# Kernel optimization log

Hardware: AMD Instinct MI355X
Metric: run time of the kernel (lower is better)

The kernel has to match this reference:

```python
import jax, jax.numpy as jnp
import numpy as np

N = 50_000      # num_nodes
E = 1_600_000   # num_edges
R = 8           # num_relations
D = 128         # hidden_dim
L = 3           # num_layers
EPS = 1e-5


def setup_inputs() -> dict:
    key = jax.random.key(0)
    ks = jax.random.split(key, 10)
    x = jnp.arange(N, dtype=jnp.int64) if jax.config.jax_enable_x64 else jnp.arange(N, dtype=jnp.int32)
    edge_index = jax.random.randint(ks[0], (2, E), 0, N)
    edge_type = jax.random.randint(ks[1], (E,), 0, R)
    emb = jax.random.normal(ks[2], (N, D), dtype=jnp.float32) * (1.0 / np.sqrt(D))
    w_rel = jax.random.normal(ks[3], (L, R, D, D), dtype=jnp.float32) * (1.0 / np.sqrt(D))
    w_root = jax.random.normal(ks[4], (L, D, D), dtype=jnp.float32) * (1.0 / np.sqrt(D))
    bias = jax.random.normal(ks[5], (L, D), dtype=jnp.float32) * 0.01
    gamma = 1.0 + 0.1 * jax.random.normal(ks[6], (L, D), dtype=jnp.float32)
    beta = 0.1 * jax.random.normal(ks[7], (L, D), dtype=jnp.float32)
    return {"x": x, "edge_index": edge_index, "edge_type": edge_type,
            "emb": emb, "w_rel": w_rel, "w_root": w_root, "bias": bias,
            "gamma": gamma, "beta": beta}


def _layer_norm(h, g, b):
    mu = jnp.mean(h, axis=-1, keepdims=True)
    var = jnp.mean(jnp.square(h - mu), axis=-1, keepdims=True)
    return (h - mu) * jax.lax.rsqrt(var + EPS) * g + b


def _rgcn_conv(h, src, dst, etype, w_rel, w_root, b):
    # PyG RGCNConv: per-relation mean aggregation of transformed neighbors + root transform + bias
    hr = jnp.einsum('nd,rdf->rnf', h, w_rel)          # [R, N, D] relation-transformed features
    msg = hr[etype, src]                               # [E, D] gather per edge
    seg = etype * N + dst                              # combined (relation, target) segment id
    sums = jax.ops.segment_sum(msg, seg, num_segments=R * N)            # [R*N, D]
    cnt = jax.ops.segment_sum(jnp.ones((msg.shape[0],), h.dtype), seg, num_segments=R * N)
    mean = sums / jnp.maximum(cnt, 1.0)[:, None]
    agg = mean.reshape(R, N, D).sum(axis=0)            # sum over relations
    return agg + h @ w_root + b


def reference(x, edge_index, edge_type, emb, w_rel, w_root, bias, gamma, beta):
    src, dst = edge_index[0], edge_index[1]
    h = emb[x]                                         # node embedding lookup
    for i in range(L):
        h_new = _rgcn_conv(h, src, dst, edge_type, w_rel[i], w_root[i], bias[i])
        h_new = jax.nn.relu(_layer_norm(h_new, gamma[i], beta[i]))
        # dropout is identity in eval/reference mode
        h = h + h_new if i > 0 else h_new
    return h
```

## Files before the change

kernel.cpp:

```cpp
#include <hip/hip_runtime.h>

#define NN 50000
#define NE 1600000
#define NR 8
#define ND 128
#define NL 3
#define RN (NR * NN)
#define LN_EPS 1e-5f
#define PADF 132

#define NBKT 196
#define BSH 11
#define STRIDE_PB 10240
#define STAGE_BYTES (NBKT * STRIDE_PB * 4)
#define BIN_BLOCKS 500
#define EPB 3200
#define I4PB 800

#define PREP_G (NN * 64)
#define PREP_W (27 * 16384)
#define PREP_TOT (PREP_G + PREP_W + NBKT)

#define WS_H    0
#define WS_ROW  14400000
#define WS_ADJ  16004096
#define WS_WB   22404096
#define WS_BIG  23288832
#define WS_NEED_NEW (23288832ULL + 9ULL * NN * 256)

typedef __attribute__((ext_vector_type(8))) short short8;
typedef __attribute__((ext_vector_type(4))) float float4v;
typedef __attribute__((ext_vector_type(4))) unsigned uint4v;

__device__ __forceinline__ float bflo(unsigned u) { return __uint_as_float(u << 16); }
__device__ __forceinline__ float bfhi(unsigned u) { return __uint_as_float(u & 0xFFFF0000u); }
__device__ __forceinline__ unsigned f2bf(float f) {
    unsigned u = __float_as_uint(f);
    return (u + 0x7FFFu + ((u >> 16) & 1u)) >> 16;
}
__device__ __forceinline__ unsigned pack2(float lo, float hi) {
    return f2bf(lo) | (f2bf(hi) << 16);
}

__global__ __launch_bounds__(256) void k_prep0(const int* __restrict__ x,
                                               const float* __restrict__ emb,
                                               const float* __restrict__ w_rel,
                                               const float* __restrict__ w_root,
                                               unsigned* __restrict__ h,
                                               unsigned short* __restrict__ wb,
                                               int* __restrict__ bcur) {
    int i = blockIdx.x * 256 + threadIdx.x;
    if (i < PREP_G) {
        int n = i >> 6, dw = i & 63;
        float2 v = *(const float2*)&emb[(size_t)x[n] * ND + 2 * dw];
        h[i] = pack2(v.x, v.y);
        return;
    }
    i -= PREP_G;
    if (i < PREP_W) {
        int m = i >> 14;
        int idx = i & 16383;
        int j = idx & 7;
        int lane = (idx >> 3) & 63;
        int ft = (idx >> 9) & 7;
        int kk = idx >> 12;
        int row = kk * 32 + (lane >> 4) * 8 + j;
        int col = ft * 16 + (lane & 15);
        const float* W = (m < 24) ? (w_rel + (size_t)m * 16384)
                                  : (w_root + (size_t)(m - 24) * 16384);
        wb[i] = (unsigned short)f2bf(W[row * ND + col]);
        return;
    }
    i -= PREP_W;
    if (i < NBKT) bcur[i] = 0;
}

__global__ __launch_bounds__(256) void k_binA(const int* __restrict__ src,
                                              const int* __restrict__ dst,
                                              const int* __restrict__ et,
                                              int* __restrict__ bcur,
                                              unsigned* __restrict__ stage) {
    __shared__ int lcnt[256];
    __shared__ int loff[256];
    __shared__ int lcur[256];
    __shared__ int sbase[256];
    __shared__ int tmp[256];
    __shared__ unsigned srt[EPB];
    __shared__ unsigned char bkt[EPB];

    int tid = threadIdx.x;
    lcnt[tid] = 0;
    __syncthreads();

    int base4 = blockIdx.x * I4PB;
    const int4* s4p = (const int4*)src;
    const int4* d4p = (const int4*)dst;
    const int4* t4p = (const int4*)et;

    for (int i4 = tid; i4 < I4PB; i4 += 256) {
        int4 d4 = d4p[base4 + i4];
        int4 t4 = t4p[base4 + i4];
        atomicAdd(&lcnt[(t4.x * NN + d4.x) >> BSH], 1);
        atomicAdd(&lcnt[(t4.y * NN + d4.y) >> BSH], 1);
        atomicAdd(&lcnt[(t4.z * NN + d4.z) >> BSH], 1);
        atomicAdd(&lcnt[(t4.w * NN + d4.w) >> BSH], 1);
    }
    __syncthreads();
    int own = lcnt[tid];
    tmp[tid] = own;
    __syncthreads();
    for (int off = 1; off < 256; off <<= 1) {
        int v = (tid >= off) ? tmp[tid - off] : 0;
        __syncthreads();
        tmp[tid] += v;
        __syncthreads();
    }
    int excl = tmp[tid] - own;
    loff[tid] = excl;
    lcur[tid] = excl;
    if (tid < NBKT) sbase[tid] = atomicAdd(&bcur[tid], own);
    __syncthreads();

    for (int i4 = tid; i4 < I4PB; i4 += 256) {
        int4 s4 = s4p[base4 + i4];
        int4 d4 = d4p[base4 + i4];
        int4 t4 = t4p[base4 + i4];
        int segs[4] = {t4.x * NN + d4.x, t4.y * NN + d4.y,
                       t4.z * NN + d4.z, t4.w * NN + d4.w};
        int srcs[4] = {s4.x, s4.y, s4.z, s4.w};
#pragma unroll
        for (int j = 0; j < 4; j++) {
            int seg = segs[j];
            int b = seg >> BSH;
            unsigned rec = ((unsigned)(seg & 2047) << 16) | (unsigned)srcs[j];
            int pos = atomicAdd(&lcur[b], 1);
            srt[pos] = rec;
            bkt[pos] = (unsigned char)b;
        }
    }
    __syncthreads();
    for (int i = tid; i < EPB; i += 256) {
        int b = bkt[i];
        stage[(size_t)b * STRIDE_PB + sbase[b] + (i - loff[b])] = srt[i];
    }
}

__global__ __launch_bounds__(256) void k_binB(const unsigned* __restrict__ stage,
                                              const int* __restrict__ bcur,
                                              int* __restrict__ rowstart,
                                              int* __restrict__ adj) {
    __shared__ int tmp[256];
    __shared__ int lcnt2[2048];
    __shared__ int loff2[2048];
    __shared__ unsigned short srt2[STRIDE_PB];
    __shared__ int gbase_s, n_s;

    int tid = threadIdx.x;
    int b = blockIdx.x;

    int bv = (tid < NBKT) ? bcur[tid] : 0;
    tmp[tid] = bv;
    __syncthreads();
    for (int off = 1; off < 256; off <<= 1) {
        int v = (tid >= off) ? tmp[tid - off] : 0;
        __syncthreads();
        tmp[tid] += v;
        __syncthreads();
    }
    if (tid == b) { gbase_s = tmp[tid] - bv; n_s = bv; }
    for (int j = tid; j < 2048; j += 256) lcnt2[j] = 0;
    __syncthreads();

    int n = n_s;
    const unsigned* sp = stage + (size_t)b * STRIDE_PB;
    for (int i = tid; i < n; i += 256)
        atomicAdd(&lcnt2[sp[i] >> 16], 1);
    __syncthreads();

    int v8[8];
    int s8 = 0;
    int base8 = tid * 8;
#pragma unroll
    for (int j = 0; j < 8; j++) { v8[j] = lcnt2[base8 + j]; s8 += v8[j]; }
    tmp[tid] = s8;
    __syncthreads();
    for (int off = 1; off < 256; off <<= 1) {
        int v = (tid >= off) ? tmp[tid - off] : 0;
        __syncthreads();
        tmp[tid] += v;
        __syncthreads();
    }
    int run = tmp[tid] - s8;
#pragma unroll
    for (int j = 0; j < 8; j++) { loff2[base8 + j] = run; run += v8[j]; }
    __syncthreads();
    for (int j = tid; j < 2048; j += 256) lcnt2[j] = loff2[j];
    __syncthreads();

    for (int i = tid; i < n; i += 256) {
        unsigned rec = sp[i];
        int pos = atomicAdd(&lcnt2[rec >> 16], 1);
        srt2[pos] = (unsigned short)(rec & 0xFFFFu);
    }
    __syncthreads();

    int gb = gbase_s;
    for (int i = tid; i < n; i += 256) adj[gb + i] = (int)srt2[i];
    int segbase = b << BSH;
    for (int j = tid; j < 2048; j += 256) {
        int seg = segbase + j;
        if (seg < RN) rowstart[seg] = gb + loff2[j];
    }
    if (b == NBKT - 1 && tid == 0) rowstart[RN] = NE;
}


__global__ __launch_bounds__(256) void k_mm(const unsigned* __restrict__ h32,
                                            const unsigned short* __restrict__ wrel,
                                            const unsigned short* __restrict__ wroot,
                                            unsigned* __restrict__ hr) {
    __shared__ uint4 SB4[2048];
    __shared__ unsigned TR[4][16][66];
    const unsigned short* SBs = (const unsigned short*)SB4;

    int tid = threadIdx.x;
    int wave = tid >> 6, lane = tid & 63;
    int quad = lane >> 4, l15 = lane & 15;
    int w0w = blockIdx.x * 64 + wave * 16;
    int gi = w0w + l15; gi = gi < NN ? gi : NN - 1;
    int pr = l15 & 1;

    const unsigned* Hrow = h32 + (size_t)gi * 64;
    short8 afr[4];
#pragma unroll
    for (int kk = 0; kk < 4; kk++)
        afr[kk] = *(const short8*)&Hrow[kk * 16 + quad * 4];

    for (int m = 0; m < 9; m++) {
        const unsigned short* W = (m < 8) ? (wrel + (size_t)m * 16384) : wroot;
        __syncthreads();
        {
            const uint4* Wg = (const uint4*)W;
#pragma unroll
            for (int i = 0; i < 8; i++) SB4[tid + 256 * i] = Wg[tid + 256 * i];
        }
        __syncthreads();

        float4v acc[8];
#pragma unroll
        for (int i = 0; i < 8; i++) acc[i] = (float4v){0.f, 0.f, 0.f, 0.f};
#pragma unroll
        for (int kk = 0; kk < 4; kk++) {
#pragma unroll
            for (int ft = 0; ft < 8; ft++) {
                short8 bf = *(const short8*)&SBs[((kk * 8 + ft) * 64 + lane) * 8];
                acc[ft] = __builtin_amdgcn_mfma_f32_16x16x32_bf16(afr[kk], bf, acc[ft], 0, 0, 0);
            }
        }

#pragma unroll
        for (int ft = 0; ft < 8; ft++) {
            float4v part;
#pragma unroll
            for (int rg = 0; rg < 4; rg++) part[rg] = __shfl_xor(acc[ft][rg], 1, 64);
            if ((ft & 1) == pr) {
                int a = l15 >> 1;
#pragma unroll
                for (int rg = 0; rg < 4; rg++) {
                    float lo = pr ? part[rg] : acc[ft][rg];
                    float hi = pr ? acc[ft][rg] : part[rg];
                    TR[wave][quad * 4 + rg][ft * 8 + a] = pack2(lo, hi);
                }
            }
        }
        unsigned* hrm = hr + (size_t)m * NN * 64;
#pragma unroll
        for (int ps = 0; ps < 4; ps++) {
            int ri = ps * 4 + quad;
            uint4 v = *(const uint4*)&TR[wave][ri][l15 * 4];
            int row = w0w + ri;
            if (row < NN)
                *(uint4*)&hrm[(size_t)row * 64 + l15 * 4] = v;
        }
    }
}

#define AGA(u)                                  \
    a0 += bflo(u.x); a1 += bfhi(u.x);           \
    a2 += bflo(u.y); a3 += bfhi(u.y);           \
    a4 += bflo(u.z); a5 += bfhi(u.z);           \
    a6 += bflo(u.w); a7 += bfhi(u.w);
#define AGC(u)                                  \
    c0 += bflo(u.x); c1 += bfhi(u.x);           \
    c2 += bflo(u.y); c3 += bfhi(u.y);           \
    c4 += bflo(u.z); c5 += bfhi(u.z);           \
    c6 += bflo(u.w); c7 += bfhi(u.w);

__global__ __launch_bounds__(256) void k_aggln(const unsigned* __restrict__ hr,
                                               unsigned* __restrict__ h32,
                                               const int* __restrict__ adj,
                                               const int* __restrict__ rowstart,
                                               const float* __restrict__ bias,
                                               const float* __restrict__ gamma,
                                               const float* __restrict__ beta,
                                               float* __restrict__ out_f,
                                               int add_res, int last) {
    int n = (blockIdx.x * 256 + threadIdx.x) >> 4;
    int l15 = threadIdx.x & 15;

    float t0 = 0.f, t1 = 0.f, t2 = 0.f, t3 = 0.f,
          t4 = 0.f, t5 = 0.f, t6 = 0.f, t7 = 0.f;

    for (int r = 0; r < NR; r++) {
        int seg = r * NN + n;
        int st = rowstart[seg], en = rowstart[seg + 1];
        st = st < 0 ? 0 : st;
        en = en > NE ? NE : en;
        const unsigned* T = hr + (size_t)r * NN * 64;

        float a0 = 0.f, a1 = 0.f, a2 = 0.f, a3 = 0.f,
              a4 = 0.f, a5 = 0.f, a6 = 0.f, a7 = 0.f;
        float c0 = 0.f, c1 = 0.f, c2 = 0.f, c3 = 0.f,
              c4 = 0.f, c5 = 0.f, c6 = 0.f, c7 = 0.f;
        int p = st;
        for (; p + 3 < en; p += 4) {
            unsigned s0 = (unsigned)adj[p],     s1 = (unsigned)adj[p + 1];
            unsigned s2 = (unsigned)adj[p + 2], s3 = (unsigned)adj[p + 3];
            s0 = s0 < NN ? s0 : NN - 1;
            s1 = s1 < NN ? s1 : NN - 1;
            s2 = s2 < NN ? s2 : NN - 1;
            s3 = s3 < NN ? s3 : NN - 1;
            uint4 u0 = *(const uint4*)&T[(size_t)s0 * 64 + l15 * 4];
            uint4 u1 = *(const uint4*)&T[(size_t)s1 * 64 + l15 * 4];
            uint4 u2 = *(const uint4*)&T[(size_t)s2 * 64 + l15 * 4];
            uint4 u3 = *(const uint4*)&T[(size_t)s3 * 64 + l15 * 4];
            AGA(u0) AGC(u1) AGA(u2) AGC(u3)
        }
        for (; p < en; p++) {
            unsigned s0 = (unsigned)adj[p];
            s0 = s0 < NN ? s0 : NN - 1;
            uint4 u0 = *(const uint4*)&T[(size_t)s0 * 64 + l15 * 4];
            AGA(u0)
        }
        int d = en - st;
        float sc = 1.0f / (float)(d > 1 ? d : 1);
        t0 += (a0 + c0) * sc; t1 += (a1 + c1) * sc;
        t2 += (a2 + c2) * sc; t3 += (a3 + c3) * sc;
        t4 += (a4 + c4) * sc; t5 += (a5 + c5) * sc;
        t6 += (a6 + c6) * sc; t7 += (a7 + c7) * sc;
    }

    {
        uint4 u = *(const uint4*)&hr[((size_t)8 * NN + n) * 64 + l15 * 4];
        t0 += bflo(u.x); t1 += bfhi(u.x);
        t2 += bflo(u.y); t3 += bfhi(u.y);
        t4 += bflo(u.z); t5 += bfhi(u.z);
        t6 += bflo(u.w); t7 += bfhi(u.w);
    }
    int f0 = 8 * l15;
    {
        float4 b0 = *(const float4*)&bias[f0];
        float4 b1 = *(const float4*)&bias[f0 + 4];
        t0 += b0.x; t1 += b0.y; t2 += b0.z; t3 += b0.w;
        t4 += b1.x; t5 += b1.y; t6 += b1.z; t7 += b1.w;
    }

    float s = t0 + t1 + t2 + t3 + t4 + t5 + t6 + t7;
#pragma unroll
    for (int off = 1; off < 16; off <<= 1) s += __shfl_xor(s, off, 64);
    float mu = s * (1.0f / ND);
    float e0 = t0 - mu, e1 = t1 - mu, e2 = t2 - mu, e3 = t3 - mu,
          e4 = t4 - mu, e5 = t5 - mu, e6 = t6 - mu, e7 = t7 - mu;
    float vs = e0 * e0 + e1 * e1 + e2 * e2 + e3 * e3 +
               e4 * e4 + e5 * e5 + e6 * e6 + e7 * e7;
#pragma unroll
    for (int off = 1; off < 16; off <<= 1) vs += __shfl_xor(vs, off, 64);
    float rr = rsqrtf(vs * (1.0f / ND) + LN_EPS);

    float4 g0 = *(const float4*)&gamma[f0];
    float4 g1 = *(const float4*)&gamma[f0 + 4];
    float4 be0 = *(const float4*)&beta[f0];
    float4 be1 = *(const float4*)&beta[f0 + 4];
    float o0 = fmaxf(e0 * rr * g0.x + be0.x, 0.0f);
    float o1 = fmaxf(e1 * rr * g0.y + be0.y, 0.0f);
    float o2 = fmaxf(e2 * rr * g0.z + be0.z, 0.0f);
    float o3 = fmaxf(e3 * rr * g0.w + be0.w, 0.0f);
    float o4 = fmaxf(e4 * rr * g1.x + be1.x, 0.0f);
    float o5 = fmaxf(e5 * rr * g1.y + be1.y, 0.0f);
    float o6 = fmaxf(e6 * rr * g1.z + be1.z, 0.0f);
    float o7 = fmaxf(e7 * rr * g1.w + be1.w, 0.0f);

    if (add_res) {
        uint4 u = *(const uint4*)&h32[(size_t)n * 64 + l15 * 4];
        o0 += bflo(u.x); o1 += bfhi(u.x);
        o2 += bflo(u.y); o3 += bfhi(u.y);
        o4 += bflo(u.z); o5 += bfhi(u.z);
        o6 += bflo(u.w); o7 += bfhi(u.w);
    }
    if (last) {
        *(float4*)&out_f[(size_t)n * ND + f0] = make_float4(o0, o1, o2, o3);
        *(float4*)&out_f[(size_t)n * ND + f0 + 4] = make_float4(o4, o5, o6, o7);
    } else {
        uint4 w;
        w.x = pack2(o0, o1); w.y = pack2(o2, o3);
        w.z = pack2(o4, o5); w.w = pack2(o6, o7);
        *(uint4*)&h32[(size_t)n * 64 + l15 * 4] = w;
    }
}


__global__ __launch_bounds__(256) void k_agg(const unsigned* __restrict__ h32,
                                             const int* __restrict__ adj,
                                             const int* __restrict__ rowstart,
                                             unsigned* __restrict__ S) {
    int q = (blockIdx.x * 256 + threadIdx.x) >> 4;
    int l15 = threadIdx.x & 15;
    int r = q / NN;
    int n = q - r * NN;
    int st = rowstart[q], en = rowstart[q + 1];
    st = st < 0 ? 0 : st;
    en = en > NE ? NE : en;
    float a0 = 0.f, a1 = 0.f, a2 = 0.f, a3 = 0.f,
          a4 = 0.f, a5 = 0.f, a6 = 0.f, a7 = 0.f;
    float c0 = 0.f, c1 = 0.f, c2 = 0.f, c3 = 0.f,
          c4 = 0.f, c5 = 0.f, c6 = 0.f, c7 = 0.f;
    int p = st;
    for (; p + 3 < en; p += 4) {
        unsigned s0 = (unsigned)adj[p],     s1 = (unsigned)adj[p + 1];
        unsigned s2 = (unsigned)adj[p + 2], s3 = (unsigned)adj[p + 3];
        s0 = s0 < NN ? s0 : NN - 1;
        s1 = s1 < NN ? s1 : NN - 1;
        s2 = s2 < NN ? s2 : NN - 1;
        s3 = s3 < NN ? s3 : NN - 1;
        uint4 u0 = *(const uint4*)&h32[(size_t)s0 * 64 + l15 * 4];
        uint4 u1 = *(const uint4*)&h32[(size_t)s1 * 64 + l15 * 4];
        uint4 u2 = *(const uint4*)&h32[(size_t)s2 * 64 + l15 * 4];
        uint4 u3 = *(const uint4*)&h32[(size_t)s3 * 64 + l15 * 4];
        AGA(u0) AGC(u1) AGA(u2) AGC(u3)
    }
    for (; p < en; p++) {
        unsigned s0 = (unsigned)adj[p];
        s0 = s0 < NN ? s0 : NN - 1;
        uint4 u0 = *(const uint4*)&h32[(size_t)s0 * 64 + l15 * 4];
        AGA(u0)
    }
    int d = en - st;
    float sc = 1.0f / (float)(d > 1 ? d : 1);
    a0 = (a0 + c0) * sc; a1 = (a1 + c1) * sc;
    a2 = (a2 + c2) * sc; a3 = (a3 + c3) * sc;
    a4 = (a4 + c4) * sc; a5 = (a5 + c5) * sc;
    a6 = (a6 + c6) * sc; a7 = (a7 + c7) * sc;
    uint4v w;
    w.x = pack2(a0, a1); w.y = pack2(a2, a3);
    w.z = pack2(a4, a5); w.w = pack2(a6, a7);
    __builtin_nontemporal_store(w, (uint4v*)&S[(size_t)n * 512 + r * 64 + l15 * 4]);
}

__global__ __launch_bounds__(256) void k_gemm(const unsigned* __restrict__ S,
                                              unsigned* __restrict__ h32,
                                              const unsigned short* __restrict__ wrel,
                                              const unsigned short* __restrict__ wroot,
                                              const float* __restrict__ bias,
                                              const float* __restrict__ gamma,
                                              const float* __restrict__ beta,
                                              float* __restrict__ out_f,
                                              int add_res, int last) {
    __shared__ char smraw[4 * 16 * PADF * 4];
    float* SLF = (float*)smraw;
    uint4* SB4 = (uint4*)smraw;
    const unsigned short* SBs = (const unsigned short*)smraw;

    int tid = threadIdx.x;
    int wave = tid >> 6, lane = tid & 63;
    int quad = lane >> 4, l15 = lane & 15;
    int w0 = blockIdx.x * 64 + wave * 16;
    int gi = w0 + l15; gi = gi < NN ? gi : NN - 1;
    float* WF = SLF + wave * 16 * PADF;

    float4v acc[8];
#pragma unroll
    for (int i = 0; i < 8; i++) acc[i] = (float4v){0.f, 0.f, 0.f, 0.f};

    const unsigned* Sr = S + (size_t)gi * 512;
    for (int r = 0; r < NR; r++) {
        short8 afr[4];
#pragma unroll
        for (int kk = 0; kk < 4; kk++)
            afr[kk] = *(const short8*)&Sr[r * 64 + kk * 16 + quad * 4];
        __syncthreads();
        {
            const uint4* Wg = (const uint4*)(wrel + (size_t)r * 16384);
#pragma unroll
            for (int i = 0; i < 8; i++) SB4[tid + 256 * i] = Wg[tid + 256 * i];
        }
        __syncthreads();
#pragma unroll
        for (int kk = 0; kk < 4; kk++) {
#pragma unroll
            for (int ft = 0; ft < 8; ft++) {
                short8 bf = *(const short8*)&SBs[((kk * 8 + ft) * 64 + lane) * 8];
                acc[ft] = __builtin_amdgcn_mfma_f32_16x16x32_bf16(afr[kk], bf, acc[ft], 0, 0, 0);
            }
        }
    }
    {
        const unsigned* Hr = h32 + (size_t)gi * 64;
        short8 afr[4];
#pragma unroll
        for (int kk = 0; kk < 4; kk++)
            afr[kk] = *(const short8*)&Hr[kk * 16 + quad * 4];
        __syncthreads();
        {
            const uint4* Wg = (const uint4*)wroot;
#pragma unroll
            for (int i = 0; i < 8; i++) SB4[tid + 256 * i] = Wg[tid + 256 * i];
        }
        __syncthreads();
#pragma unroll
        for (int kk = 0; kk < 4; kk++) {
#pragma unroll
            for (int ft = 0; ft < 8; ft++) {
                short8 bf = *(const short8*)&SBs[((kk * 8 + ft) * 64 + lane) * 8];
                acc[ft] = __builtin_amdgcn_mfma_f32_16x16x32_bf16(afr[kk], bf, acc[ft], 0, 0, 0);
            }
        }
    }
    __syncthreads();

#pragma unroll
    for (int ft = 0; ft < 8; ft++)
#pragma unroll
        for (int rg = 0; rg < 4; rg++)
            WF[(quad * 4 + rg) * PADF + ft * 16 + l15] = acc[ft][rg];

    float2 bia = *(const float2*)&bias[2 * lane];
    float2 gam = *(const float2*)&gamma[2 * lane];
    float2 bet = *(const float2*)&beta[2 * lane];

    for (int i = 0; i < 16; i++) {
        int g = w0 + i;
        if (g >= NN) continue;
        float v0 = WF[i * PADF + 2 * lane] + bia.x;
        float v1 = WF[i * PADF + 2 * lane + 1] + bia.y;
        float s = v0 + v1;
#pragma unroll
        for (int off = 32; off > 0; off >>= 1) s += __shfl_xor(s, off, 64);
        float mu = s * (1.0f / ND);
        float e0 = v0 - mu, e1 = v1 - mu;
        float vs = e0 * e0 + e1 * e1;
#pragma unroll
        for (int off = 32; off > 0; off >>= 1) vs += __shfl_xor(vs, off, 64);
        float rr = rsqrtf(vs * (1.0f / ND) + LN_EPS);
        float o0 = fmaxf(e0 * rr * gam.x + bet.x, 0.0f);
        float o1 = fmaxf(e1 * rr * gam.y + bet.y, 0.0f);
        if (add_res) {
            unsigned u = h32[(size_t)g * 64 + lane];
            o0 += bflo(u);
            o1 += bfhi(u);
        }
        if (last) {
            *(float2*)&out_f[(size_t)g * ND + 2 * lane] = make_float2(o0, o1);
        } else {
            h32[(size_t)g * 64 + lane] = pack2(o0, o1);
        }
    }
}

extern "C" void kernel_launch(void* const* d_in, const int* in_sizes, int n_in,
                              void* d_out, int out_size, void* d_ws, size_t ws_size,
                              hipStream_t stream) {
    const int*   x      = (const int*)d_in[0];
    const int*   ei     = (const int*)d_in[1];
    const int*   et     = (const int*)d_in[2];
    const float* emb    = (const float*)d_in[3];
    const float* w_rel  = (const float*)d_in[4];
    const float* w_root = (const float*)d_in[5];
    const float* bias   = (const float*)d_in[6];
    const float* gamma  = (const float*)d_in[7];
    const float* beta   = (const float*)d_in[8];
    float* out = (float*)d_out;

    char* ws = (char*)d_ws;
    unsigned* h        = (unsigned*)(ws + WS_H);
    int*      rowstart = (int*)     (ws + WS_ROW);
    int*      adj      = (int*)     (ws + WS_ADJ);
    unsigned short* wb = (unsigned short*)(ws + WS_WB);
    unsigned* big      = (unsigned*)(ws + WS_BIG);
    unsigned* stage    = big;
    int*      bcur     = (int*)     (ws + WS_BIG + STAGE_BYTES);

    const int* src = ei;
    const int* dst = ei + NE;

    k_prep0<<<(PREP_TOT + 255) / 256, 256, 0, stream>>>(x, emb, w_rel, w_root,
                                                        h, wb, bcur);
    k_binA<<<BIN_BLOCKS, 256, 0, stream>>>(src, dst, et, bcur, stage);
    k_binB<<<NBKT, 256, 0, stream>>>(stage, bcur, rowstart, adj);

    if (ws_size >= WS_NEED_NEW) {
        for (int l = 0; l < NL; l++) {
            k_mm<<<(NN + 63) / 64, 256, 0, stream>>>(
                h, wb + (size_t)l * 8 * 16384, wb + (size_t)(24 + l) * 16384, big);
            k_aggln<<<NN * 16 / 256, 256, 0, stream>>>(
                big, h, adj, rowstart,
                bias + l * ND, gamma + l * ND, beta + l * ND,
                out, l > 0, l == NL - 1);
        }
    } else {
        for (int l = 0; l < NL; l++) {
            k_agg<<<RN * 16 / 256, 256, 0, stream>>>(h, adj, rowstart, big);
            k_gemm<<<(NN + 63) / 64, 256, 0, stream>>>(
                big, h,
                wb + (size_t)l * 8 * 16384, wb + (size_t)(24 + l) * 16384,
                bias + l * ND, gamma + l * ND, beta + l * ND,
                out, l > 0, l == NL - 1);
        }
    }
}
```

Measured before the change: 510.8 us.

## Merge prep with binning and first-layer GEMM with CSR finalize to cut launches

Folds the embedding/weight conversion blocks into the edge-binning kernel and runs the second binning pass alongside the first layer's relation GEMM in one launch, so independent work overlaps and kernel launches drop. Staging now lives in the output buffer with bcur zeroed by memset, and bounds clamps on source indices in the aggregation loops are removed with a 2-wide tail added. This adds overflow guards on stage indices and relies on input indices being in range.

```diff
diff --git a/kernel.cpp b/kernel.cpp
--- a/kernel.cpp
+++ b/kernel.cpp
@@ -12,17 +12,19 @@
 #define NBKT 196
 #define BSH 11
 #define STRIDE_PB 10240
-#define STAGE_BYTES (NBKT * STRIDE_PB * 4)
 #define BIN_BLOCKS 500
 #define EPB 3200
 #define I4PB 800
+#define MM_BLOCKS ((NN + 63) / 64)
 
 #define PREP_G (NN * 64)
 #define PREP_W (27 * 16384)
-#define PREP_TOT (PREP_G + PREP_W + NBKT)
+#define PREP_TOT (PREP_G + PREP_W)
+#define PREP_BLOCKS ((PREP_TOT + 255) / 256)
 
 #define WS_H    0
 #define WS_ROW  14400000
+#define WS_BCUR 16000064
 #define WS_ADJ  16004096
 #define WS_WB   22404096
 #define WS_BIG  23288832
@@ -42,44 +44,17 @@
     return f2bf(lo) | (f2bf(hi) << 16);
 }
 
-__global__ __launch_bounds__(256) void k_prep0(const int* __restrict__ x,
-                                               const float* __restrict__ emb,
-                                               const float* __restrict__ w_rel,
-                                               const float* __restrict__ w_root,
-                                               unsigned* __restrict__ h,
-                                               unsigned short* __restrict__ wb,
-                                               int* __restrict__ bcur) {
-    int i = blockIdx.x * 256 + threadIdx.x;
-    if (i < PREP_G) {
-        int n = i >> 6, dw = i & 63;
-        float2 v = *(const float2*)&emb[(size_t)x[n] * ND + 2 * dw];
-        h[i] = pack2(v.x, v.y);
-        return;
-    }
-    i -= PREP_G;
-    if (i < PREP_W) {
-        int m = i >> 14;
-        int idx = i & 16383;
-        int j = idx & 7;
-        int lane = (idx >> 3) & 63;
-        int ft = (idx >> 9) & 7;
-        int kk = idx >> 12;
-        int row = kk * 32 + (lane >> 4) * 8 + j;
-        int col = ft * 16 + (lane & 15);
-        const float* W = (m < 24) ? (w_rel + (size_t)m * 16384)
-                                  : (w_root + (size_t)(m - 24) * 16384);
-        wb[i] = (unsigned short)f2bf(W[row * ND + col]);
-        return;
-    }
-    i -= PREP_W;
-    if (i < NBKT) bcur[i] = 0;
-}
-
-__global__ __launch_bounds__(256) void k_binA(const int* __restrict__ src,
-                                              const int* __restrict__ dst,
-                                              const int* __restrict__ et,
-                                              int* __restrict__ bcur,
-                                              unsigned* __restrict__ stage) {
+__global__ __launch_bounds__(256) void k_prepbin(const int* __restrict__ x,
+                                                 const float* __restrict__ emb,
+                                                 const float* __restrict__ w_rel,
+                                                 const float* __restrict__ w_root,
+                                                 const int* __restrict__ src,
+                                                 const int* __restrict__ dst,
+                                                 const int* __restrict__ et,
+                                                 unsigned* __restrict__ h,
+                                                 unsigned short* __restrict__ wb,
+                                                 int* __restrict__ bcur,
+                                                 unsigned* __restrict__ stage) {
     __shared__ int lcnt[256];
     __shared__ int loff[256];
     __shared__ int lcur[256];
@@ -89,6 +64,31 @@
     __shared__ unsigned char bkt[EPB];
 
     int tid = threadIdx.x;
+    if (blockIdx.x >= BIN_BLOCKS) {
+        int i = (blockIdx.x - BIN_BLOCKS) * 256 + tid;
+        if (i < PREP_G) {
+            int n = i >> 6, dw = i & 63;
+            float2 v = *(const float2*)&emb[(size_t)x[n] * ND + 2 * dw];
+            h[i] = pack2(v.x, v.y);
+            return;
+        }
+        i -= PREP_G;
+        if (i < PREP_W) {
+            int m = i >> 14;
+            int idx = i & 16383;
+            int j = idx & 7;
+            int lane = (idx >> 3) & 63;
+            int ft = (idx >> 9) & 7;
+            int kk = idx >> 12;
+            int row = kk * 32 + (lane >> 4) * 8 + j;
+            int col = ft * 16 + (lane & 15);
+            const float* W = (m < 24) ? (w_rel + (size_t)m * 16384)
+                                      : (w_root + (size_t)(m - 24) * 16384);
+            wb[i] = (unsigned short)f2bf(W[row * ND + col]);
+        }
+        return;
+    }
+
     lcnt[tid] = 0;
     __syncthreads();
 
@@ -141,23 +141,19 @@
     __syncthreads();
     for (int i = tid; i < EPB; i += 256) {
         int b = bkt[i];
-        stage[(size_t)b * STRIDE_PB + sbase[b] + (i - loff[b])] = srt[i];
-    }
-}
-
-__global__ __launch_bounds__(256) void k_binB(const unsigned* __restrict__ stage,
-                                              const int* __restrict__ bcur,
-                                              int* __restrict__ rowstart,
-                                              int* __restrict__ adj) {
-    __shared__ int tmp[256];
-    __shared__ int lcnt2[2048];
-    __shared__ int loff2[2048];
-    __shared__ unsigned short srt2[STRIDE_PB];
-    __shared__ int gbase_s, n_s;
-
-    int tid = threadIdx.x;
-    int b = blockIdx.x;
-
+        int idx = sbase[b] + (i - loff[b]);
+        if (idx < STRIDE_PB)
+            stage[(size_t)b * STRIDE_PB + idx] = srt[i];
+    }
+}
+
+__device__ __forceinline__ void binB_body(const unsigned* __restrict__ stage,
+                                          const int* __restrict__ bcur,
+                                          int* __restrict__ rowstart,
+                                          int* __restrict__ adj,
+                                          int b, int tid,
+                                          int* tmp, int* lcnt2, int* loff2,
+                                          unsigned short* srt2, int* misc) {
     int bv = (tid < NBKT) ? bcur[tid] : 0;
     tmp[tid] = bv;
     __syncthreads();
@@ -167,11 +163,12 @@
         tmp[tid] += v;
         __syncthreads();
     }
-    if (tid == b) { gbase_s = tmp[tid] - bv; n_s = bv; }
+    if (tid == b) { misc[0] = tmp[tid] - bv; misc[1] = bv; }
     for (int j = tid; j < 2048; j += 256) lcnt2[j] = 0;
     __syncthreads();
 
-    int n = n_s;
+    int n = misc[1];
+    n = n < STRIDE_PB ? n : STRIDE_PB;
     const unsigned* sp = stage + (size_t)b * STRIDE_PB;
     for (int i = tid; i < n; i += 256)
         atomicAdd(&lcnt2[sp[i] >> 16], 1);
@@ -204,7 +201,7 @@
     }
     __syncthreads();
 
-    int gb = gbase_s;
+    int gb = misc[0];
     for (int i = tid; i < n; i += 256) adj[gb + i] = (int)srt2[i];
     int segbase = b << BSH;
     for (int j = tid; j < 2048; j += 256) {
@@ -214,75 +211,122 @@
     if (b == NBKT - 1 && tid == 0) rowstart[RN] = NE;
 }
 
+typedef unsigned TRarr[16][66];
+
+__device__ __forceinline__ void mm_body(const unsigned* __restrict__ h32,
+                                        const unsigned short* __restrict__ wrel,
+                                        const unsigned short* __restrict__ wroot,
+                                        unsigned* __restrict__ hr,
+                                        int mb, int tid,
+                                        uint4* SB4, TRarr* TRp) {
+    const unsigned short* SBs = (const unsigned short*)SB4;
+    int wave = tid >> 6, lane = tid & 63;
+    int quad = lane >> 4, l15 = lane & 15;
+    int w0w = mb * 64 + wave * 16;
+    int gi = w0w + l15; gi = gi < NN ? gi : NN - 1;
+    int pr = l15 & 1;
+
+    const unsigned* Hrow = h32 + (size_t)gi * 64;
+    short8 afr[4];
+#pragma unroll
+    for (int kk = 0; kk < 4; kk++)
+        afr[kk] = *(const short8*)&Hrow[kk * 16 + quad * 4];
+
+    for (int m = 0; m < 9; m++) {
+        const unsigned short* W = (m < 8) ? (wrel + (size_t)m * 16384) : wroot;
+        __syncthreads();
+        {
+            const uint4* Wg = (const uint4*)W;
+#pragma unroll
+            for (int i = 0; i < 8; i++) SB4[tid + 256 * i] = Wg[tid + 256 * i];
+        }
+        __syncthreads();
+
+        float4v acc[8];
+#pragma unroll
+        for (int i = 0; i < 8; i++) acc[i] = (float4v){0.f, 0.f, 0.f, 0.f};
+#pragma unroll
+        for (int kk = 0; kk < 4; kk++) {
+#pragma unroll
+            for (int ft = 0; ft < 8; ft++) {
+                short8 bf = *(const short8*)&SBs[((kk * 8 + ft) * 64 + lane) * 8];
+                acc[ft] = __builtin_amdgcn_mfma_f32_16x16x32_bf16(afr[kk], bf, acc[ft], 0, 0, 0);
+            }
+        }
+
+#pragma unroll
+        for (int ft = 0; ft < 8; ft++) {
+            float4v part;
+#pragma unroll
+            for (int rg = 0; rg < 4; rg++) part[rg] = __shfl_xor(acc[ft][rg], 1, 64);
+            if ((ft & 1) == pr) {
+                int a = l15 >> 1;
+#pragma unroll
+                for (int rg = 0; rg < 4; rg++) {
+                    float lo = pr ? part[rg] : acc[ft][rg];
+                    float hi = pr ? acc[ft][rg] : part[rg];
+                    TRp[wave][quad * 4 + rg][ft * 8 + a] = pack2(lo, hi);
+                }
+            }
+        }
+        unsigned* hrm = hr + (size_t)m * NN * 64;
+#pragma unroll
+        for (int ps = 0; ps < 4; ps++) {
+            int ri = ps * 4 + quad;
+            uint4 v = *(const uint4*)&TRp[wave][ri][l15 * 4];
+            int row = w0w + ri;
+            if (row < NN)
+                *(uint4*)&hrm[(size_t)row * 64 + l15 * 4] = v;
+        }
+    }
+}
+
+__global__ __launch_bounds__(256) void k_binB_mm(const unsigned* __restrict__ stage,
+                                                 const int* __restrict__ bcur,
+                                                 int* __restrict__ rowstart,
+                                                 int* __restrict__ adj,
+                                                 const unsigned* __restrict__ h32,
+                                                 const unsigned short* __restrict__ wrel,
+                                                 const unsigned short* __restrict__ wroot,
+                                                 unsigned* __restrict__ hr) {
+    __shared__ uint4 SMEM[3104];
+    int tid = threadIdx.x;
+    if (blockIdx.x < NBKT) {
+        int* tmp = (int*)SMEM;
+        int* lcnt2 = (int*)SMEM + 256;
+        int* loff2 = (int*)SMEM + 2304;
+        unsigned short* srt2 = (unsigned short*)((int*)SMEM + 4352);
+        int* misc = (int*)SMEM + 9472;
+        binB_body(stage, bcur, rowstart, adj, blockIdx.x, tid,
+                  tmp, lcnt2, loff2, srt2, misc);
+    } else {
+        mm_body(h32, wrel, wroot, hr, blockIdx.x - NBKT, tid,
+                SMEM, (TRarr*)(SMEM + 2048));
+    }
+}
+
+__global__ __launch_bounds__(256) void k_binB(const unsigned* __restrict__ stage,
+                                              const int* __restrict__ bcur,
+                                              int* __restrict__ rowstart,
+                                              int* __restrict__ adj) {
+    __shared__ uint4 SMEM[2369];
+    int tid = threadIdx.x;
+    int* tmp = (int*)SMEM;
+    int* lcnt2 = (int*)SMEM + 256;
+    int* loff2 = (int*)SMEM + 2304;
+    unsigned short* srt2 = (unsigned short*)((int*)SMEM + 4352);
+    int* misc = (int*)SMEM + 9472;
+    binB_body(stage, bcur, rowstart, adj, blockIdx.x, tid,
+              tmp, lcnt2, loff2, srt2, misc);
+}
 
 __global__ __launch_bounds__(256) void k_mm(const unsigned* __restrict__ h32,
                                             const unsigned short* __restrict__ wrel,
                                             const unsigned short* __restrict__ wroot,
                                             unsigned* __restrict__ hr) {
-    __shared__ uint4 SB4[2048];
-    __shared__ unsigned TR[4][16][66];
-    const unsigned short* SBs = (const unsigned short*)SB4;
-
-    int tid = threadIdx.x;
-    int wave = tid >> 6, lane = tid & 63;
-    int quad = lane >> 4, l15 = lane & 15;
-    int w0w = blockIdx.x * 64 + wave * 16;
-    int gi = w0w + l15; gi = gi < NN ? gi : NN - 1;
-    int pr = l15 & 1;
-
-    const unsigned* Hrow = h32 + (size_t)gi * 64;
-    short8 afr[4];
-#pragma unroll
-    for (int kk = 0; kk < 4; kk++)
-        afr[kk] = *(const short8*)&Hrow[kk * 16 + quad * 4];
-
-    for (int m = 0; m < 9; m++) {
-        const unsigned short* W = (m < 8) ? (wrel + (size_t)m * 16384) : wroot;
-        __syncthreads();
-        {
-            const uint4* Wg = (const uint4*)W;
-#pragma unroll
-            for (int i = 0; i < 8; i++) SB4[tid + 256 * i] = Wg[tid + 256 * i];
-        }
-        __syncthreads();
-
-        float4v acc[8];
-#pragma unroll
-        for (int i = 0; i < 8; i++) acc[i] = (float4v){0.f, 0.f, 0.f, 0.f};
-#pragma unroll
-        for (int kk = 0; kk < 4; kk++) {
-#pragma unroll
-            for (int ft = 0; ft < 8; ft++) {
-                short8 bf = *(const short8*)&SBs[((kk * 8 + ft) * 64 + lane) * 8];
-                acc[ft] = __builtin_amdgcn_mfma_f32_16x16x32_bf16(afr[kk], bf, acc[ft], 0, 0, 0);
-            }
-        }
-
-#pragma unroll
-        for (int ft = 0; ft < 8; ft++) {
-            float4v part;
-#pragma unroll
-            for (int rg = 0; rg < 4; rg++) part[rg] = __shfl_xor(acc[ft][rg], 1, 64);
-            if ((ft & 1) == pr) {
-                int a = l15 >> 1;
-#pragma unroll
-                for (int rg = 0; rg < 4; rg++) {
-                    float lo = pr ? part[rg] : acc[ft][rg];
-                    float hi = pr ? acc[ft][rg] : part[rg];
-                    TR[wave][quad * 4 + rg][ft * 8 + a] = pack2(lo, hi);
-                }
-            }
-        }
-        unsigned* hrm = hr + (size_t)m * NN * 64;
-#pragma unroll
-        for (int ps = 0; ps < 4; ps++) {
-            int ri = ps * 4 + quad;
-            uint4 v = *(const uint4*)&TR[wave][ri][l15 * 4];
-            int row = w0w + ri;
-            if (row < NN)
-                *(uint4*)&hrm[(size_t)row * 64 + l15 * 4] = v;
-        }
-    }
+    __shared__ uint4 SMEM[3104];
+    mm_body(h32, wrel, wroot, hr, blockIdx.x, threadIdx.x,
+            SMEM, (TRarr*)(SMEM + 2048));
 }
 
 #define AGA(u)                                  \
@@ -326,19 +370,20 @@
         for (; p + 3 < en; p += 4) {
             unsigned s0 = (unsigned)adj[p],     s1 = (unsigned)adj[p + 1];
             unsigned s2 = (unsigned)adj[p + 2], s3 = (unsigned)adj[p + 3];
-            s0 = s0 < NN ? s0 : NN - 1;
-            s1 = s1 < NN ? s1 : NN - 1;
-            s2 = s2 < NN ? s2 : NN - 1;
-            s3 = s3 < NN ? s3 : NN - 1;
             uint4 u0 = *(const uint4*)&T[(size_t)s0 * 64 + l15 * 4];
             uint4 u1 = *(const uint4*)&T[(size_t)s1 * 64 + l15 * 4];
             uint4 u2 = *(const uint4*)&T[(size_t)s2 * 64 + l15 * 4];
             uint4 u3 = *(const uint4*)&T[(size_t)s3 * 64 + l15 * 4];
             AGA(u0) AGC(u1) AGA(u2) AGC(u3)
         }
-        for (; p < en; p++) {
+        for (; p + 1 < en; p += 2) {
+            unsigned s0 = (unsigned)adj[p], s1 = (unsigned)adj[p + 1];
+            uint4 u0 = *(const uint4*)&T[(size_t)s0 * 64 + l15 * 4];
+            uint4 u1 = *(const uint4*)&T[(size_t)s1 * 64 + l15 * 4];
+            AGA(u0) AGC(u1)
+        }
+        if (p < en) {
             unsigned s0 = (unsigned)adj[p];
-            s0 = s0 < NN ? s0 : NN - 1;
             uint4 u0 = *(const uint4*)&T[(size_t)s0 * 64 + l15 * 4];
             AGA(u0)
         }
@@ -428,10 +473,6 @@
     for (; p + 3 < en; p += 4) {
         unsigned s0 = (unsigned)adj[p],     s1 = (unsigned)adj[p + 1];
         unsigned s2 = (unsigned)adj[p + 2], s3 = (unsigned)adj[p + 3];
-        s0 = s0 < NN ? s0 : NN - 1;
-        s1 = s1 < NN ? s1 : NN - 1;
-        s2 = s2 < NN ? s2 : NN - 1;
-        s3 = s3 < NN ? s3 : NN - 1;
         uint4 u0 = *(const uint4*)&h32[(size_t)s0 * 64 + l15 * 4];
         uint4 u1 = *(const uint4*)&h32[(size_t)s1 * 64 + l15 * 4];
         uint4 u2 = *(const uint4*)&h32[(size_t)s2 * 64 + l15 * 4];
@@ -440,7 +481,6 @@
     }
     for (; p < en; p++) {
         unsigned s0 = (unsigned)adj[p];
-        s0 = s0 < NN ? s0 : NN - 1;
         uint4 u0 = *(const uint4*)&h32[(size_t)s0 * 64 + l15 * 4];
         AGA(u0)
     }
@@ -583,30 +623,37 @@
     char* ws = (char*)d_ws;
     unsigned* h        = (unsigned*)(ws + WS_H);
     int*      rowstart = (int*)     (ws + WS_ROW);
+    int*      bcur     = (int*)     (ws + WS_BCUR);
     int*      adj      = (int*)     (ws + WS_ADJ);
     unsigned short* wb = (unsigned short*)(ws + WS_WB);
     unsigned* big      = (unsigned*)(ws + WS_BIG);
-    unsigned* stage    = big;
-    int*      bcur     = (int*)     (ws + WS_BIG + STAGE_BYTES);
+    unsigned* stage    = (unsigned*)d_out;
 
     const int* src = ei;
     const int* dst = ei + NE;
 
-    k_prep0<<<(PREP_TOT + 255) / 256, 256, 0, stream>>>(x, emb, w_rel, w_root,
-                                                        h, wb, bcur);
-    k_binA<<<BIN_BLOCKS, 256, 0, stream>>>(src, dst, et, bcur, stage);
-    k_binB<<<NBKT, 256, 0, stream>>>(stage, bcur, rowstart, adj);
+    hipMemsetAsync(bcur, 0, NBKT * sizeof(int), stream);
+
+    k_prepbin<<<BIN_BLOCKS + PREP_BLOCKS, 256, 0, stream>>>(
+        x, emb, w_rel, w_root, src, dst, et, h, wb, bcur, stage);
 
     if (ws_size >= WS_NEED_NEW) {
-        for (int l = 0; l < NL; l++) {
-            k_mm<<<(NN + 63) / 64, 256, 0, stream>>>(
+        k_binB_mm<<<NBKT + MM_BLOCKS, 256, 0, stream>>>(
+            stage, bcur, rowstart, adj,
+            h, wb, wb + (size_t)24 * 16384, big);
+        k_aggln<<<NN * 16 / 256, 256, 0, stream>>>(
+            big, h, adj, rowstart,
+            bias, gamma, beta, out, 0, 0);
+        for (int l = 1; l < NL; l++) {
+            k_mm<<<MM_BLOCKS, 256, 0, stream>>>(
                 h, wb + (size_t)l * 8 * 16384, wb + (size_t)(24 + l) * 16384, big);
             k_aggln<<<NN * 16 / 256, 256, 0, stream>>>(
                 big, h, adj, rowstart,
                 bias + l * ND, gamma + l * ND, beta + l * ND,
-                out, l > 0, l == NL - 1);
+                out, 1, l == NL - 1);
         }
     } else {
+        k_binB<<<NBKT, 256, 0, stream>>>(stage, bcur, rowstart, adj);
         for (int l = 0; l < NL; l++) {
             k_agg<<<RN * 16 / 256, 256, 0, stream>>>(h, adj, rowstart, big);
             k_gemm<<<(NN + 63) / 64, 256, 0, stream>>>(
```

After: 502.6 us. Within noise of the previous version (-1.6%).
